# Kernel optimization log

Measured on AMD Instinct MI355X. Metric: run time of the kernel, lower is better.

Reference implementation:

```python
import jax, jax.numpy as jnp
import numpy as np

B, S, D, V = 2, 4096, 2048, 32000
H, HD = 16, 128          # heads, head dim (H*HD == D)
BS = 16                  # block_size
N_ANCH = 128             # num_anchors (static: loss_mask=ones guarantees enough valid positions)
MASK_ID = 31999
DFF = 8192


def rms(x, w, eps=1e-6):
    return x * jax.lax.rsqrt(jnp.mean(x * x, axis=-1, keepdims=True) + eps) * w


def rope(x, pos):
    # x: (..., L, H, hd), pos: (..., L)
    hd = x.shape[-1]
    inv = 1.0 / (10000.0 ** (jnp.arange(0, hd, 2, dtype=jnp.float32) / hd))
    ang = pos[..., None, None].astype(jnp.float32) * inv  # (..., L, 1, hd/2)
    cos, sin = jnp.cos(ang), jnp.sin(ang)
    x1, x2 = x[..., : hd // 2], x[..., hd // 2 :]
    return jnp.concatenate([x1 * cos - x2 * sin, x2 * cos + x1 * sin], axis=-1).astype(x.dtype)


def setup_inputs() -> dict:
    key = jax.random.key(0)
    ks = jax.random.split(key, 12)
    s = 0.02
    return {
        "input_ids": jax.random.randint(ks[0], (B, S), 0, V, dtype=jnp.int32),
        "hidden_states": jax.random.normal(ks[1], (B, S, D), dtype=jnp.float32),
        "loss_mask": jnp.ones((B, S), dtype=jnp.float32),
        "rand_vals": jax.random.uniform(ks[2], (B, S - BS + 1), dtype=jnp.float32),
        "embed_table": jax.random.normal(ks[3], (V, D), dtype=jnp.float32) * s,
        "lm_head_w": jax.random.normal(ks[4], (V, D), dtype=jnp.float32) * s,
        "wq": jax.random.normal(ks[5], (D, D), dtype=jnp.float32) * s,
        "wk": jax.random.normal(ks[6], (D, D), dtype=jnp.float32) * s,
        "wv": jax.random.normal(ks[7], (D, D), dtype=jnp.float32) * s,
        "wo": jax.random.normal(ks[8], (D, D), dtype=jnp.float32) * s,
        "w_gate": jax.random.normal(ks[9], (D, DFF), dtype=jnp.float32) * s,
        "w_up": jax.random.normal(ks[10], (D, DFF), dtype=jnp.float32) * s,
        "w_down": jax.random.normal(ks[11], (DFF, D), dtype=jnp.float32) * s,
        "norm_attn": jnp.ones((D,), dtype=jnp.float32),
        "norm_mlp": jnp.ones((D,), dtype=jnp.float32),
        "norm_out": jnp.ones((D,), dtype=jnp.float32),
        "norm_chs": jnp.ones((D,), dtype=jnp.float32),
    }


def reference(input_ids, hidden_states, loss_mask, rand_vals, embed_table, lm_head_w,
              wq, wk, wv, wo, w_gate, w_up, w_down, norm_attn, norm_mlp, norm_out, norm_chs):
    max_anchor = S - BS
    # ---- anchor sampling: random permutation of valid positions via argsort of rand ----
    valid = loss_mask[:, : max_anchor + 1] > 0.5                       # (B, max_anchor+1)
    valid_counts = valid.sum(axis=1)
    idx = jnp.arange(max_anchor + 1, dtype=jnp.int32)
    masked_idx = jnp.where(valid, idx[None, :], S + 1)
    rv = jnp.where(valid, rand_vals, 2.0)
    order = jnp.argsort(rv, axis=1)
    gathered = jnp.take_along_axis(masked_idx, order, axis=1)
    anchors = jnp.sort(gathered[:, :N_ANCH], axis=1)                   # (B, N)
    keep = jnp.arange(N_ANCH)[None, :] < jnp.minimum(valid_counts, N_ANCH)[:, None]
    anchors = jnp.where(keep, anchors, 0)
    # ---- noise embedding: anchor token at block start, mask token elsewhere ----
    anchor_tok = jnp.take_along_axis(input_ids, jnp.clip(anchors, 0, S - 1), axis=1)
    first_tok = jnp.where(keep, anchor_tok, MASK_ID)
    noise_ids = jnp.full((B, N_ANCH, BS), MASK_ID, dtype=jnp.int32).at[:, :, 0].set(first_tok)
    x = embed_table[noise_ids]                                         # (B,N,BS,D)
    # ---- CHS context hidden: target hidden at anchor-1 ----
    ctx_pos = jnp.maximum(anchors - 1, 0)
    ctx = jnp.take_along_axis(hidden_states, ctx_pos[:, :, None], axis=1)  # (B,N,D)
    # ---- block-diagonal attention: per-block kv = [CHS_i | draft block i] (kv_len=1+BS) ----
    pos_q = anchors[:, :, None] + jnp.arange(BS)[None, None, :]        # (B,N,BS)
    pos_kv = jnp.concatenate([ctx_pos[:, :, None], pos_q], axis=2)     # (B,N,1+BS)
    hq = rms(x, norm_attn)
    hc = rms(ctx, norm_chs)[:, :, None, :]
    kv_in = jnp.concatenate([hc, hq], axis=2)                          # (B,N,1+BS,D)
    q = rope((hq @ wq).reshape(B, N_ANCH, BS, H, HD), pos_q)
    k = rope((kv_in @ wk).reshape(B, N_ANCH, 1 + BS, H, HD), pos_kv)
    v = (kv_in @ wv).reshape(B, N_ANCH, 1 + BS, H, HD)
    scores = jnp.einsum('bnqhd,bnkhd->bnhqk', q, k) * (1.0 / HD ** 0.5)
    attn = jax.nn.softmax(scores, axis=-1)
    out = jnp.einsum('bnhqk,bnkhd->bnqhd', attn, v).reshape(B, N_ANCH, BS, D) @ wo
    out = out * keep[:, :, None, None].astype(out.dtype)               # invalid blocks fully masked
    x = x + out
    h = rms(x, norm_mlp)
    x = x + (jax.nn.silu(h @ w_gate) * (h @ w_up)) @ w_down
    h_out = rms(x, norm_out)
    logits = h_out @ lm_head_w.T                                       # (B,N,BS,V)
    # ---- block-wise CE loss ----
    label_idx = anchors[:, :, None] + jnp.arange(BS)[None, None, :]
    valid_label = label_idx < S
    safe = jnp.minimum(label_idx, S - 1)
    targets = jnp.take_along_axis(jnp.broadcast_to(input_ids[:, None, :], (B, N_ANCH, S)), safe, axis=2)
    lm_g = jnp.take_along_axis(jnp.broadcast_to(loss_mask[:, None, :], (B, N_ANCH, S)), safe, axis=2)
    weight = (keep[:, :, None] & valid_label).astype(jnp.float32)
    weight = weight * (jnp.arange(BS) > 0)[None, None, :].astype(jnp.float32) * lm_g
    logp = jax.nn.log_softmax(logits, axis=-1)
    tok_logp = jnp.take_along_axis(logp, targets[..., None].astype(jnp.int32), axis=-1)[..., 0]
    loss = -(tok_logp * weight).sum() / (weight.sum() + 1e-6)
    pred = jnp.argmax(logits, axis=-1)
    accuracy = ((pred == targets) & (weight > 0.5)).sum().astype(jnp.float32) / (weight.sum() + 1e-6)
    return loss, accuracy
```

## Files before the change

### kernel.cpp

```cpp
#include <hip/hip_runtime.h>
#include <math.h>

typedef unsigned short u16;
typedef unsigned char u8;
typedef short v8s __attribute__((ext_vector_type(8)));
typedef u16   v4u __attribute__((ext_vector_type(4)));
typedef float v4f __attribute__((ext_vector_type(4)));
typedef int   v2i __attribute__((ext_vector_type(2)));
typedef int   v4i __attribute__((ext_vector_type(4)));

#define DEVFN static __device__ __forceinline__

constexpr int cB = 2, cS = 4096, cD = 2048, cV = 32000, cH = 16, cHD = 128;
constexpr int cBS = 16, cNA = 128, cMASK = 31999, cDFF = 8192;
constexpr int NCAND = cS - cBS + 1;
constexpr int MTOK  = cB * cNA * cBS;
constexpr int MKV   = cB * cNA * 17;
constexpr int NCH   = cV / 128;
constexpr int NCH2  = cV / 256;

constexpr int EPI_BF16 = 0, EPI_SILU = 1, EPI_OEMB = 2, EPI_DOWNACC = 3, EPI_STATS = 4, EPI_GLU = 5;
constexpr int ASRC_BF16 = 0, ASRC_RMS = 1, ASRC_AOMAP = 2;

struct RmsSrc {
// ... 160 lines not shown
  long i = ((long)blockIdx.x * 256 + threadIdx.x) * 8;
  long stride = (long)gridDim.x * 256 * 8;
  for (; i < n; i += stride) {
    v4f a = *(const v4f*)(in + i), b = *(const v4f*)(in + i + 4);
    v2i pk;
    pk[0] = pack4fp8(a[0] * scale, a[1] * scale, a[2] * scale, a[3] * scale);
    pk[1] = pack4fp8(b[0] * scale, b[1] * scale, b[2] * scale, b[3] * scale);
    *(v2i*)(out + perm8(i)) = pk;
  }
}

__global__ void k_cvt8(const u16* __restrict__ in, u8* __restrict__ out, long n) {
  long i = ((long)blockIdx.x * 256 + threadIdx.x) * 8;
  long stride = (long)gridDim.x * 256 * 8;
  for (; i < n; i += stride) {
    v8s a = *(const v8s*)(in + i);
    v2i pk;
    pk[0] = pack4fp8(bf2f((u16)a[0]), bf2f((u16)a[1]), bf2f((u16)a[2]), bf2f((u16)a[3]));
    pk[1] = pack4fp8(bf2f((u16)a[4]), bf2f((u16)a[5]), bf2f((u16)a[6]), bf2f((u16)a[7]));
    *(v2i*)(out + perm8(i)) = pk;
  }
}

__global__ void k_tconv(const float* __restrict__ W, u16* __restrict__ WT, int K, int N) {
  __shared__ u16 t[64][72];
  int n0 = blockIdx.x * 64, k0 = blockIdx.y * 64;
  int tid = threadIdx.x;
  int c4 = (tid & 15) * 4, r0 = tid >> 4;
  #pragma unroll
  for (int rr = 0; rr < 64; rr += 16) {
    int k = r0 + rr;
    v4f v = *(const v4f*)(W + (size_t)(k0 + k) * N + n0 + c4);
    #pragma unroll
    for (int e = 0; e < 4; ++e) t[c4 + e][k] = f2bf(v[e]);
  }
  __syncthreads();
  int n = tid >> 2, kq = (tid & 3) * 16;
  v8s o0, o1;
  #pragma unroll
  for (int e = 0; e < 8; ++e) { o0[e] = (short)t[n][kq + e]; o1[e] = (short)t[n][kq + 8 + e]; }
  *(v8s*)(WT + (size_t)(n0 + n) * K + k0 + kq) = o0;
  *(v8s*)(WT + (size_t)(n0 + n) * K + k0 + kq + 8) = o1;
}

__global__ void k_tconv8(const float* __restrict__ W, u8* __restrict__ WT8,
                         int K, int N, int goff, float scale) {
  __shared__ float tf[64][65];
  int n0 = blockIdx.x * 64, k0 = blockIdx.y * 64;
  int tid = threadIdx.x;
  int c4 = (tid & 15) * 4, r0 = tid >> 4;
  #pragma unroll
  for (int rr = 0; rr < 64; rr += 16) {
    int k = r0 + rr;
    v4f v = *(const v4f*)(W + (size_t)(k0 + k) * N + n0 + c4);
    #pragma unroll
    for (int e = 0; e < 4; ++e) tf[c4 + e][k] = v[e];
  }
  __syncthreads();
  int n = tid >> 2, kq = (tid & 3) * 16;
  int gn = n0 + n;
  size_t rout = (goff >= 0) ? (((size_t)(gn >> 4) << 5) + goff + (gn & 15)) : (size_t)gn;
  long base = (long)rout * K + k0 + kq;
  v2i p0, p1;
  p0[0] = pack4fp8(tf[n][kq + 0] * scale, tf[n][kq + 1] * scale, tf[n][kq + 2] * scale, tf[n][kq + 3] * scale);
  p0[1] = pack4fp8(tf[n][kq + 4] * scale, tf[n][kq + 5] * scale, tf[n][kq + 6] * scale, tf[n][kq + 7] * scale);
  p1[0] = pack4fp8(tf[n][kq + 8] * scale, tf[n][kq + 9] * scale, tf[n][kq + 10] * scale, tf[n][kq + 11] * scale);
  p1[1] = pack4fp8(tf[n][kq + 12] * scale, tf[n][kq + 13] * scale, tf[n][kq + 14] * scale, tf[n][kq + 15] * scale);
// ... 94 lines not shown
    __builtin_amdgcn_s_setprio(0);
    __builtin_amdgcn_s_barrier();

    if (t + 2 < NT) stageA(t + 2, 1);
    __builtin_amdgcn_s_setprio(1);
    #pragma unroll
    for (int mi = 0; mi < 4; ++mi)
      #pragma unroll
      for (int ni = 0; ni < 4; ++ni)
        acc[mi + 4][ni] = __builtin_amdgcn_mfma_f32_16x16x32_fp8_fp8(fa[mi + 4].ll[1], fb[ni].ll[1], acc[mi + 4][ni], 0, 0, 0);
    __builtin_amdgcn_s_setprio(0);
    if (t + 2 < NT) { asm volatile("s_waitcnt vmcnt(4)" ::: "memory"); }
    else            { asm volatile("s_waitcnt vmcnt(0)" ::: "memory"); }
    __builtin_amdgcn_s_barrier();
  }
  asm volatile("s_waitcnt vmcnt(0)" ::: "memory");

  #pragma unroll
  for (int mi = 0; mi < 8; ++mi)
    #pragma unroll
    for (int ni = 0; ni < 4; ++ni)
      acc[mi][ni] *= 0.015625f;

  if constexpr (EPI == EPI_GLU) {
    #pragma unroll
    for (int mi = 0; mi < 8; ++mi)
      #pragma unroll
      for (int np = 0; np < 2; ++np)
        #pragma unroll
        for (int r = 0; r < 4; ++r) {
          int grow = m0 + wm * 128 + mi * 16 + lq * 4 + r;
          int gcol = (n0 >> 1) + wn * 32 + np * 16 + lc;
          float g = acc[mi][2 * np][r];
          float u = acc[mi][2 * np + 1][r];
          C8[perm8((size_t)grow * ldc + gcol)] = f2fp8(u * g / (1.0f + __expf(-g)));
        }
    return;
  } else {
    float* s_mx = (float*)lds8;
    float* s_sm = (float*)(lds8 + 4096);
    int*   s_ax = (int*)(lds8 + 8192);
    __syncthreads();
    #pragma unroll
    for (int mi = 0; mi < 8; ++mi) {
      #pragma unroll
      for (int r = 0; r < 4; ++r) {
        float v0 = acc[mi][0][r], v1 = acc[mi][1][r], v2 = acc[mi][2][r], v3 = acc[mi][3][r];
        float mx = v0; int ax = lc;
        if (v1 > mx) { mx = v1; ax = 16 + lc; }
        if (v2 > mx) { mx = v2; ax = 32 + lc; }
        if (v3 > mx) { mx = v3; ax = 48 + lc; }
        #pragma unroll
        for (int off = 1; off < 16; off <<= 1) {
          float om = __shfl_xor(mx, off); int oa = __shfl_xor(ax, off);
          if (om > mx || (om == mx && oa < ax)) { mx = om; ax = oa; }
        }
        float se = __expf(v0 - mx) + __expf(v1 - mx) + __expf(v2 - mx) + __expf(v3 - mx);
        #pragma unroll
        for (int off = 1; off < 16; off <<= 1) se += __shfl_xor(se, off);
        if (lc == 0) {
          int row = wm * 128 + mi * 16 + lq * 4 + r;
          s_mx[row * 4 + wn] = mx; s_sm[row * 4 + wn] = se; s_ax[row * 4 + wn] = wn * 64 + ax;
        }
      }
    }
    __syncthreads();
    if (tid < 256) {
      float gm = s_mx[tid * 4]; int ga = s_ax[tid * 4];
      #pragma unroll
      for (int w = 1; w < 4; ++w) {
        float m = s_mx[tid * 4 + w];
        if (m > gm) { gm = m; ga = s_ax[tid * 4 + w]; }
      }
      float gs = 0.f;
      #pragma unroll
      for (int w = 0; w < 4; ++w) gs += s_sm[tid * 4 + w] * __expf(s_mx[tid * 4 + w] - gm);
      v4f rec; rec[0] = gm; rec[1] = gs; rec[2] = __int_as_float(n0 + ga); rec[3] = 0.f;
      partials[(size_t)(m0 + tid) * nch + blockIdx.y] = rec;
    }
  }
}

template <int EPI>
__launch_bounds__(256, 4)
__global__ void k_gemm9(const u8* __restrict__ A8, const u8* __restrict__ B8,
                        u16* __restrict__ Cbf, float* __restrict__ Cf32,
                        const int* __restrict__ keepArr, RmsSrc rs,
                        int K, int ldb, int ldc) {
  __shared__ __align__(16) u8 lds8[32768];
  const int tid = threadIdx.x;
  const int lane = tid & 63, wid = tid >> 6;
  const int wm = wid >> 1, wn = wid & 1;
  const int lc = lane & 15, lq = lane >> 4;
  const int m0 = blockIdx.x * 128, n0 = blockIdx.y * 128;

  const u8* srcA[2]; const u8* srcB[2];
  #pragma unroll
  for (int i = 0; i < 2; ++i) {
    int ci = i * 256 + tid;
    int r = ci >> 2;
    int logc = (ci & 3) ^ ((r >> 1) & 3);
    srcA[i] = A8 + (size_t)(m0 + r) * K + logc * 16;
// ... 60 lines not shown
  }

  #pragma unroll
  for (int mi = 0; mi < 4; ++mi)
    #pragma unroll
    for (int ni = 0; ni < 4; ++ni)
      #pragma unroll
      for (int r = 0; r < 4; ++r) {
        int grow = m0 + wm * 64 + mi * 16 + lq * 4 + r;
        int gcol = n0 + wn * 64 + ni * 16 + lc;
        size_t idx = (size_t)grow * ldc + gcol;
        float vv = acc[mi][ni][r] * 0.015625f;
        if constexpr (EPI == EPI_BF16) {
          Cbf[idx] = f2bf(vv);
        } else if constexpr (EPI == EPI_OEMB) {
          int t_ = grow & 15, bn = grow >> 4;
          int tok = (t_ == 0) ? rs.ftok[bn] : cMASK;
          float kf = (float)keepArr[bn];
          Cf32[idx] = rs.emb[(size_t)tok * cD + gcol] + vv * kf;
        } else {
          Cf32[idx] += vv;
        }
      }
}

template <int ASRC, int BLAYOUT, int EPI>
__launch_bounds__(256)
__global__ void k_gemm(const u16* __restrict__ Abf, const float* __restrict__ Bw,
                       u16* Cbf, float* Cf32, const u16* Gaux,
                       const int* __restrict__ keepArr, v4f* __restrict__ partials,
                       RmsSrc rs, int K, int ldb, int ldc) {
  __shared__ __align__(16) u16 As[128][40];
  __shared__ __align__(16) u16 Bs[128][40];
  const int tid = threadIdx.x;
  const int m0 = blockIdx.x * 128, n0 = blockIdx.y * 128;
  const int lane = tid & 63, wid = tid >> 6;
  const int wm = wid >> 1, wn = wid & 1;
  const int lc = lane & 15, lk8 = (lane >> 4) * 8;
  const int srow = tid >> 2, sk8 = (tid & 3) * 8;
  v4f acc[4][4];
  #pragma unroll
  for (int i = 0; i < 4; ++i)
    #pragma unroll
    for (int j = 0; j < 4; ++j) acc[i][j] = (v4f){0.f, 0.f, 0.f, 0.f};

  for (int kt = 0; kt < K; kt += 32) {
    __syncthreads();
    for (int mm = srow; mm < 128; mm += 64) {
      if constexpr (ASRC == ASRC_BF16) {
        *(v8s*)&As[mm][sk8] = *(const v8s*)(Abf + (size_t)(m0 + mm) * K + kt + sk8);
      } else if constexpr (ASRC == ASRC_AOMAP) {
        int m = m0 + mm, bn = m >> 4, t = m & 15;
        *(v8s*)&As[mm][sk8] = *(const v8s*)(Abf + (size_t)(bn * 17 + 1 + t) * K + kt + sk8);
      } else {
        int R = m0 + mm;
        int j = R % 17, bn = R / 17, b = bn >> 7;
        const float* src; const float* nw;
        if (j == 0) { src = rs.hs + ((size_t)b * cS + rs.cpos[bn]) * cD; nw = rs.nchs; }
        else {
          int tok = (j == 1) ? rs.ftok[bn] : cMASK;
          src = rs.emb + (size_t)tok * cD; nw = rs.nattn;
        }
        float inv = rs.rowinv[R];
        const v4f* sp = (const v4f*)(src + kt + sk8);
        const v4f* np_ = (const v4f*)(nw + kt + sk8);
        v4f s0 = sp[0], s1 = sp[1], w0 = np_[0], w1 = np_[1];
        v8s pk;
        #pragma unroll
        for (int e = 0; e < 4; ++e) pk[e] = (short)f2bf(s0[e] * inv * w0[e]);
        #pragma unroll
        for (int e = 0; e < 4; ++e) pk[4 + e] = (short)f2bf(s1[e] * inv * w1[e]);
        *(v8s*)&As[mm][sk8] = pk;
      }
    }
    if constexpr (BLAYOUT == 1) {
      for (int nn = srow; nn < 128; nn += 64) {
        const v4f* bp = (const v4f*)(Bw + (size_t)(n0 + nn) * ldb + kt + sk8);
        v4f b0 = bp[0], b1 = bp[1];
        v8s pk;
        #pragma unroll
        for (int e = 0; e < 4; ++e) { pk[e] = (short)f2bf(b0[e]); pk[4 + e] = (short)f2bf(b1[e]); }
        *(v8s*)&Bs[nn][sk8] = pk;
      }
    } else {
      const int bn_ = tid & 127, kq = tid >> 7;
      for (int kk = kq; kk < 8; kk += 2) {
        const int k4 = kk * 4;
        const float* bp = Bw + (size_t)(kt + k4) * ldb + n0 + bn_;
        v4u pk;
        #pragma unroll
        for (int e = 0; e < 4; ++e) pk[e] = f2bf(bp[(size_t)e * ldb]);
        *(v4u*)&Bs[bn_][k4] = pk;
      }
    }
    __syncthreads();
    v8s af[4], bf_[4];
    #pragma unroll
    for (int i = 0; i < 4; ++i) af[i] = *(const v8s*)&As[wm * 64 + i * 16 + lc][lk8];
    #pragma unroll
    for (int i = 0; i < 4; ++i) bf_[i] = *(const v8s*)&Bs[wn * 64 + i * 16 + lc][lk8];
    #pragma unroll
    for (int mi = 0; mi < 4; ++mi)
      #pragma unroll
      for (int ni = 0; ni < 4; ++ni)
        acc[mi][ni] = __builtin_amdgcn_mfma_f32_16x16x32_bf16(af[mi], bf_[ni], acc[mi][ni], 0, 0, 0);
  }

  if constexpr (EPI == EPI_STATS) {
    __shared__ float s_mx[128][2], s_sm[128][2];
    __shared__ int s_ax[128][2];
    #pragma unroll
    for (int mi = 0; mi < 4; ++mi) {
      #pragma unroll
      for (int r = 0; r < 4; ++r) {
        float v0 = acc[mi][0][r], v1 = acc[mi][1][r], v2 = acc[mi][2][r], v3 = acc[mi][3][r];
        float mx = v0; int ax = lc;
        if (v1 > mx) { mx = v1; ax = 16 + lc; }
        if (v2 > mx) { mx = v2; ax = 32 + lc; }
        if (v3 > mx) { mx = v3; ax = 48 + lc; }
        #pragma unroll
        for (int off = 1; off < 16; off <<= 1) {
          float om = __shfl_xor(mx, off); int oa = __shfl_xor(ax, off);
          if (om > mx || (om == mx && oa < ax)) { mx = om; ax = oa; }
        }
        float se = __expf(v0 - mx) + __expf(v1 - mx) + __expf(v2 - mx) + __expf(v3 - mx);
        #pragma unroll
        for (int off = 1; off < 16; off <<= 1) se += __shfl_xor(se, off);
        if (lc == 0) {
          int lr = wm * 64 + mi * 16 + (lane >> 4) * 4 + r;
          s_mx[lr][wn] = mx; s_sm[lr][wn] = se; s_ax[lr][wn] = wn * 64 + ax;
        }
      }
    }
    __syncthreads();
    if (tid < 128) {
      float ma = s_mx[tid][0], mb = s_mx[tid][1];
      float gm = fmaxf(ma, mb);
      float gs = s_sm[tid][0] * __expf(ma - gm) + s_sm[tid][1] * __expf(mb - gm);
      int ga = (ma >= mb) ? s_ax[tid][0] : s_ax[tid][1];
      v4f rec; rec[0] = gm; rec[1] = gs; rec[2] = __int_as_float(n0 + ga); rec[3] = 0.f;
      partials[(size_t)(m0 + tid) * NCH + blockIdx.y] = rec;
    }
    return;
  } else {
    #pragma unroll
    for (int mi = 0; mi < 4; ++mi)
      #pragma unroll
      for (int ni = 0; ni < 4; ++ni)
        #pragma unroll
        for (int r = 0; r < 4; ++r) {
          int grow = m0 + wm * 64 + mi * 16 + (lane >> 4) * 4 + r;
          int gcol = n0 + wn * 64 + ni * 16 + lc;
          size_t idx = (size_t)grow * ldc + gcol;
          float vv = acc[mi][ni][r];
          if constexpr (EPI == EPI_BF16) {
            Cbf[idx] = f2bf(vv);
          } else if constexpr (EPI == EPI_SILU) {
            float g = bf2f(Gaux[idx]);
            Cbf[idx] = f2bf(vv * g / (1.0f + __expf(-g)));
          } else if constexpr (EPI == EPI_OEMB) {
            int t = grow & 15, bn = grow >> 4;
            int tok = (t == 0) ? rs.ftok[bn] : cMASK;
            float kf = (float)keepArr[bn];
            Cf32[idx] = rs.emb[(size_t)tok * cD + gcol] + vv * kf;
          } else {
            Cf32[idx] += vv;
          }
        }
  }
}

__global__ void k_rope(u16* __restrict__ qb, u16* __restrict__ kb,
                       const int* __restrict__ anchors, const int* __restrict__ cpos) {
  int r = blockIdx.x;
  int which = (r >= MKV);
  int rr = which ? r - MKV : r;
  int j = rr % 17, bn = rr / 17;
  if (!which && j == 0) return;
  u16* buf = which ? kb : qb;
  int pos = (which && j == 0) ? cpos[bn] : (anchors[bn] + j - 1);
  float fp = (float)pos;
  for (int p = threadIdx.x; p < cH * 64; p += 256) {
    int h = p >> 6, i = p & 63;
    size_t base = (size_t)rr * cD + h * cHD;
    float x1 = bf2f(buf[base + i]);
    float x2 = bf2f(buf[base + 64 + i]);
    float freq = powf(10000.0f, -((float)(2 * i)) / 128.0f);
    float ang = fp * freq;
    float sn = sinf(ang), cn = cosf(ang);
    buf[base + i]      = f2bf(x1 * cn - x2 * sn);
    buf[base + 64 + i] = f2bf(x2 * cn + x1 * sn);
  }
// ... 15 lines not shown
    vs[r][d] = bf2f(vb[((size_t)(bn * 17 + r)) * cD + h * cHD + d]);
  }
  __syncthreads();
  for (int e = lane; e < 16 * 17; e += 64) {
    int qi = e / 17, ki = e % 17;
    float s = 0.f;
    for (int d = 0; d < 128; ++d) s += qs[qi][d] * ks[ki][d];
    ps[qi][ki] = s * 0.08838834764831845f;
  }
  __syncthreads();
  if (lane < 16) {
    float m = -3e38f;
    for (int kk = 0; kk < 17; ++kk) m = fmaxf(m, ps[lane][kk]);
    float s = 0.f;
    for (int kk = 0; kk < 17; ++kk) { float e_ = __expf(ps[lane][kk] - m); ps[lane][kk] = e_; s += e_; }
    float is = 1.0f / s;
    for (int kk = 0; kk < 17; ++kk) ps[lane][kk] *= is;
  }
  __syncthreads();
  for (int e = lane; e < 16 * 128; e += 64) {
    int qi = e >> 7, d = e & 127;
    float s = 0.f;
    for (int kk = 0; kk < 17; ++kk) s += ps[qi][kk] * vs[kk][d];
    if (ao8) ao8[perm8((size_t)(bn * 16 + qi) * cD + h * cHD + d)] = f2fp8(s);
    else     qb[((size_t)(bn * 17 + 1 + qi)) * cD + h * cHD + d] = f2bf(s);
  }
}

__global__ void k_tgt(const u16* __restrict__ hout, const float* __restrict__ Wlm,
                      const int* __restrict__ ids, const int* __restrict__ anchors,
                      int* __restrict__ tgt_tok, float* __restrict__ tgt_logit) {
  int w = threadIdx.x >> 6, lane = threadIdx.x & 63;
  int m = blockIdx.x * 4 + w;
  int bn = m >> 4, t = m & 15, b = bn / cNA;
  int label = anchors[bn] + t;
  int sl = (label < cS - 1) ? label : (cS - 1);
  int tok = ids[(size_t)b * cS + sl];
  const u16* hr = hout + (size_t)m * cD;
  const float* wr = Wlm + (size_t)tok * cD;
  float s = 0.f;
  for (int d = lane; d < cD; d += 64) s += bf2f(hr[d]) * wr[d];
  s = waveSum(s);
  if (lane == 0) { tgt_tok[m] = tok; tgt_logit[m] = s; }
}

__global__ void k_combine(const v4f* __restrict__ partials, const int* __restrict__ tgt_tok,
                          const float* __restrict__ tgt_logit, const int* __restrict__ keepArr,
                          const int* __restrict__ anchors, const float* __restrict__ lmask,
// ... 47 lines not shown
  for (int m = tid; m < MTOK; m += 256) {
    swl += tokOut[m * 4 + 0];
    sw  += tokOut[m * 4 + 1];
    sm  += tokOut[m * 4 + 2];
  }
  swl = waveSum(swl); sw = waveSum(sw); sm = waveSum(sm);
  __shared__ float r0[4], r1[4], r2[4];
  int lane = tid & 63, w = tid >> 6;
  if (lane == 0) { r0[w] = swl; r1[w] = sw; r2[w] = sm; }
  __syncthreads();
  if (tid == 0) {
    float a = r0[0] + r0[1] + r0[2] + r0[3];
    float b = r1[0] + r1[1] + r1[2] + r1[3];
    float c = r2[0] + r2[1] + r2[2] + r2[3];
    float denom = b + 1e-6f;
    float loss = -a / denom;
    float acc  = c / denom;
    if (b == 0.0f) loss = -300.0f;
    outp[0] = loss;
    outp[1] = acc;
  }
}

__global__ void k_heartbeat(float* outp) {
  if (threadIdx.x == 0) { outp[0] = -55.0f; outp[1] = -55.0f; }
}
__global__ void k_sentinel(float* outp) {
  if (threadIdx.x == 0) { outp[0] = -777.0f; outp[1] = -777.0f; }
}

extern "C" void kernel_launch(void* const* d_in, const int* in_sizes, int n_in,
                              void* d_out, int out_size, void* d_ws, size_t ws_size,
                              hipStream_t stream) {
  const int*   ids   = (const int*)  d_in[0];
  const float* hs    = (const float*)d_in[1];
  const float* lmask = (const float*)d_in[2];
  const float* rv    = (const float*)d_in[3];
  const float* emb   = (const float*)d_in[4];
  const float* wlm   = (const float*)d_in[5];
  const float* wq    = (const float*)d_in[6];
  const float* wk    = (const float*)d_in[7];
  const float* wv    = (const float*)d_in[8];
  const float* wo    = (const float*)d_in[9];
  const float* wg    = (const float*)d_in[10];
  const float* wu    = (const float*)d_in[11];
  const float* wd    = (const float*)d_in[12];
  const float* nattn = (const float*)d_in[13];
  const float* nmlp  = (const float*)d_in[14];
  const float* nout  = (const float*)d_in[15];
  const float* nchs  = (const float*)d_in[16];
  (void)in_sizes; (void)n_in; (void)out_size;

  float* outp = (float*)d_out;
  k_heartbeat<<<dim3(1), 64, 0, stream>>>(outp);

  char* wsb = (char*)d_ws;
  size_t off = 0;
  auto alloc = [&](size_t bytes) -> void* {
    void* p = wsb + off;
    off = (off + bytes + 255) & ~(size_t)255;
    return p;
  };
  int*   anchors = (int*)  alloc((size_t)cB * cNA * 4);
  int*   keepA   = (int*)  alloc((size_t)cB * cNA * 4);
  int*   ftok    = (int*)  alloc((size_t)cB * cNA * 4);
  int*   cpos    = (int*)  alloc((size_t)cB * cNA * 4);
  int*   self    = (int*)  alloc((size_t)cB * NCAND * 4);
  float* rowinv  = (float*)alloc((size_t)MKV * 4);
  int*   ttok    = (int*)  alloc((size_t)MTOK * 4);
  float* tlogit  = (float*)alloc((size_t)MTOK * 4);
  float* tokOut  = (float*)alloc((size_t)MTOK * 4 * 4);

  const size_t szQ  = (size_t)MKV * cD * 2;
  const size_t szX  = (size_t)MTOK * cD * 4;
  u16* qb = (u16*)alloc(szQ);
  const size_t a1off = off;

// ... 51 lines not shown
    k_gemm9<EPI_OEMB><<<dim3(MTOK / 128, cD / 128), 256, 0, stream>>>(
        ao8, wo8, nullptr, xb, keepA, rs, cD, cD, cD);

    k_rms<<<dim3(MTOK), 256, 0, stream>>>(xb, nmlp, hb);
    k_cvt8<<<dim3(1024), 256, 0, stream>>>(hb, h8m, (long)MTOK * cD);

    k_tconv8<<<dim3(128, 32), 256, 0, stream>>>(wg, wgu8, cD, cDFF, 0, 64.0f);
    k_tconv8<<<dim3(128, 32), 256, 0, stream>>>(wu, wgu8, cD, cDFF, 16, 64.0f);
    k_tconv8<<<dim3(32, 128), 256, 0, stream>>>(wd, wd8, cDFF, cD, -1, 64.0f);

    for (int cb = 0; cb < cDFF; cb += 4096) {
      k_gemm8<EPI_GLU><<<dim3(MTOK / 256, 32), 512, 0, stream>>>(
          h8m, wgu8 + (size_t)cb * 2 * cD, cbuf8, nullptr, cD, 4096, 0);
      k_gemm9<EPI_DOWNACC><<<dim3(MTOK / 128, cD / 128), 256, 0, stream>>>(
          cbuf8, wd8 + cb, nullptr, xb, nullptr, rs, 4096, cDFF, cD);
    }

    k_rms<<<dim3(MTOK), 256, 0, stream>>>(xb, nout, houtb);

    k_tgt<<<dim3(MTOK / 4), 256, 0, stream>>>(houtb, wlm, ids, anchors, ttok, tlogit);

    k_cvt8 <<<dim3(1024), 256, 0, stream>>>(houtb, h8, (long)MTOK * cD);
    k_conv8<<<dim3(2048), 256, 0, stream>>>(wlm, wlm8, (long)cV * cD, 64.0f);
    k_gemm8<EPI_STATS><<<dim3(MTOK / 256, NCH2), 512, 0, stream>>>(
        h8, wlm8, nullptr, parts, cD, 0, NCH2);

    k_combine<<<dim3(MTOK), 256, 0, stream>>>(parts, ttok, tlogit, keepA, anchors, lmask, tokOut, NCH2);
    k_final  <<<dim3(1), 256, 0, stream>>>(tokOut, outp);
    return;
  }

  const int cwopts[4] = {4096, 2048, 1024, 512};
  int CW = 0;
  for (int ci = 0; ci < 4; ++ci) {
    int cw = cwopts[ci];
    size_t cbufsz = (size_t)MTOK * cw * 2;
    size_t s1 = 2 * szQ;
    size_t s2 = szX + cbufsz;
    size_t sz = s1 > s2 ? s1 : s2;
    size_t pmin = (size_t)MTOK * NCH * 16;
    if (pmin > sz) sz = pmin;
    if (a1off + sz <= ws_size) { CW = cw; break; }
  }
  if (CW == 0) { k_sentinel<<<dim3(1), 64, 0, stream>>>(outp); return; }

  u16*   kb    = (u16*)(wsb + a1off);
  u16*   vb    = (u16*)(wsb + a1off + szQ);
  float* xb    = (float*)(wsb + a1off);
  u16*   cbuf  = (u16*)(wsb + a1off + szX);
  v4f*   parts = (v4f*)(wsb + a1off);
  u16*   hb    = qb;
  u16*   houtb = qb;

  k_rowinv<<<dim3(MKV), 256, 0, stream>>>(hs, emb, ftok, cpos, rowinv);

  k_gemm<ASRC_RMS, 0, EPI_BF16><<<dim3(MKV / 128, cD / 128), 256, 0, stream>>>(
      nullptr, wq, qb, nullptr, nullptr, nullptr, nullptr, rs, cD, cD, cD);
  k_gemm<ASRC_RMS, 0, EPI_BF16><<<dim3(MKV / 128, cD / 128), 256, 0, stream>>>(
      nullptr, wk, kb, nullptr, nullptr, nullptr, nullptr, rs, cD, cD, cD);
  k_gemm<ASRC_RMS, 0, EPI_BF16><<<dim3(MKV / 128, cD / 128), 256, 0, stream>>>(
      nullptr, wv, vb, nullptr, nullptr, nullptr, nullptr, rs, cD, cD, cD);

  k_rope<<<dim3(2 * MKV), 256, 0, stream>>>(qb, kb, anchors, cpos);
  k_attn<<<dim3(cB * cNA * cH), 64, 0, stream>>>(qb, kb, vb, nullptr);

  k_gemm<ASRC_AOMAP, 0, EPI_OEMB><<<dim3(MTOK / 128, cD / 128), 256, 0, stream>>>(
      qb, wo, nullptr, xb, nullptr, keepA, nullptr, rs, cD, cD, cD);

  k_rms<<<dim3(MTOK), 256, 0, stream>>>(xb, nmlp, hb);

  for (int cb = 0; cb < cDFF; cb += CW) {
    k_gemm<ASRC_BF16, 0, EPI_BF16><<<dim3(MTOK / 128, CW / 128), 256, 0, stream>>>(
        hb, wg + cb, cbuf, nullptr, nullptr, nullptr, nullptr, rs, cD, cDFF, CW);
    k_gemm<ASRC_BF16, 0, EPI_SILU><<<dim3(MTOK / 128, CW / 128), 256, 0, stream>>>(
        hb, wu + cb, cbuf, nullptr, cbuf, nullptr, nullptr, rs, cD, cDFF, CW);
    k_gemm<ASRC_BF16, 0, EPI_DOWNACC><<<dim3(MTOK / 128, cD / 128), 256, 0, stream>>>(
        cbuf, wd + (size_t)cb * cD, nullptr, xb, nullptr, nullptr, nullptr, rs, CW, cD, cD);
  }

  k_rms<<<dim3(MTOK), 256, 0, stream>>>(xb, nout, houtb);

  k_tgt<<<dim3(MTOK / 4), 256, 0, stream>>>(houtb, wlm, ids, anchors, ttok, tlogit);
  k_gemm<ASRC_BF16, 1, EPI_STATS><<<dim3(MTOK / 128, cV / 128), 256, 0, stream>>>(
      houtb, wlm, nullptr, nullptr, nullptr, nullptr, parts, rs, cD, cD, 0);

  k_combine<<<dim3(MTOK), 256, 0, stream>>>(parts, ttok, tlogit, keepA, anchors, lmask, tokOut, NCH);
  k_final  <<<dim3(1), 256, 0, stream>>>(tokOut, outp);
}
```

Before: 1.443 ms.

## Add 512x256-tile FP8 LM-head GEMM kernel with fused softmax stats; drop bf16 fallback

Adds a dedicated LM-head GEMM kernel that uses 512x256 output tiles per 512-thread block (16x4 accumulator fragments per wave) with a double-buffered 96KB LDS pipeline and interleaved staging. It keeps the fused per-chunk max/sum-exp/argmax epilogue, and the EPI_STATS path moves out of the generic FP8 GEMM, which now only handles GLU. The larger tile is meant to raise operand reuse and cut global/LDS traffic for the vocab projection. In exchange it runs one block per CU with high register pressure and fewer blocks in the grid. The unused bf16 fallback path, the heartbeat kernel and dead helpers are removed.

New measurement: 2.431 ms. +68.4%, slower.

```diff
diff --git a/kernel.cpp b/kernel.cpp
--- a/kernel.cpp
+++ b/kernel.cpp
@@ -206,27 +206,6 @@
   }
 }
 
-__global__ void k_tconv(const float* __restrict__ W, u16* __restrict__ WT, int K, int N) {
-  __shared__ u16 t[64][72];
-  int n0 = blockIdx.x * 64, k0 = blockIdx.y * 64;
-  int tid = threadIdx.x;
-  int c4 = (tid & 15) * 4, r0 = tid >> 4;
-  #pragma unroll
-  for (int rr = 0; rr < 64; rr += 16) {
-    int k = r0 + rr;
-    v4f v = *(const v4f*)(W + (size_t)(k0 + k) * N + n0 + c4);
-    #pragma unroll
-    for (int e = 0; e < 4; ++e) t[c4 + e][k] = f2bf(v[e]);
-  }
-  __syncthreads();
-  int n = tid >> 2, kq = (tid & 3) * 16;
-  v8s o0, o1;
-  #pragma unroll
-  for (int e = 0; e < 8; ++e) { o0[e] = (short)t[n][kq + e]; o1[e] = (short)t[n][kq + 8 + e]; }
-  *(v8s*)(WT + (size_t)(n0 + n) * K + k0 + kq) = o0;
-  *(v8s*)(WT + (size_t)(n0 + n) * K + k0 + kq + 8) = o1;
-}
-
 __global__ void k_tconv8(const float* __restrict__ W, u8* __restrict__ WT8,
                          int K, int N, int goff, float scale) {
   __shared__ float tf[64][65];
@@ -367,62 +346,195 @@
     for (int ni = 0; ni < 4; ++ni)
       acc[mi][ni] *= 0.015625f;
 
-  if constexpr (EPI == EPI_GLU) {
-    #pragma unroll
-    for (int mi = 0; mi < 8; ++mi)
-      #pragma unroll
-      for (int np = 0; np < 2; ++np)
-        #pragma unroll
-        for (int r = 0; r < 4; ++r) {
-          int grow = m0 + wm * 128 + mi * 16 + lq * 4 + r;
-          int gcol = (n0 >> 1) + wn * 32 + np * 16 + lc;
-          float g = acc[mi][2 * np][r];
-          float u = acc[mi][2 * np + 1][r];
-          C8[perm8((size_t)grow * ldc + gcol)] = f2fp8(u * g / (1.0f + __expf(-g)));
-        }
-    return;
-  } else {
-    float* s_mx = (float*)lds8;
-    float* s_sm = (float*)(lds8 + 4096);
-    int*   s_ax = (int*)(lds8 + 8192);
-    __syncthreads();
-    #pragma unroll
-    for (int mi = 0; mi < 8; ++mi) {
+  #pragma unroll
+  for (int mi = 0; mi < 8; ++mi)
+    #pragma unroll
+    for (int np = 0; np < 2; ++np)
       #pragma unroll
       for (int r = 0; r < 4; ++r) {
-        float v0 = acc[mi][0][r], v1 = acc[mi][1][r], v2 = acc[mi][2][r], v3 = acc[mi][3][r];
-        float mx = v0; int ax = lc;
-        if (v1 > mx) { mx = v1; ax = 16 + lc; }
-        if (v2 > mx) { mx = v2; ax = 32 + lc; }
-        if (v3 > mx) { mx = v3; ax = 48 + lc; }
-        #pragma unroll
-        for (int off = 1; off < 16; off <<= 1) {
-          float om = __shfl_xor(mx, off); int oa = __shfl_xor(ax, off);
-          if (om > mx || (om == mx && oa < ax)) { mx = om; ax = oa; }
-        }
-        float se = __expf(v0 - mx) + __expf(v1 - mx) + __expf(v2 - mx) + __expf(v3 - mx);
-        #pragma unroll
-        for (int off = 1; off < 16; off <<= 1) se += __shfl_xor(se, off);
-        if (lc == 0) {
-          int row = wm * 128 + mi * 16 + lq * 4 + r;
-          s_mx[row * 4 + wn] = mx; s_sm[row * 4 + wn] = se; s_ax[row * 4 + wn] = wn * 64 + ax;
-        }
+        int grow = m0 + wm * 128 + mi * 16 + lq * 4 + r;
+        int gcol = (n0 >> 1) + wn * 32 + np * 16 + lc;
+        float g = acc[mi][2 * np][r];
+        float u = acc[mi][2 * np + 1][r];
+        C8[perm8((size_t)grow * ldc + gcol)] = f2fp8(u * g / (1.0f + __expf(-g)));
+      }
+  (void)partials; (void)nch;
+}
+
+__launch_bounds__(512, 1)
+__global__ void k_gemm10(const u8* __restrict__ A8, const u8* __restrict__ B8,
+                         v4f* __restrict__ partials, int K, int nch) {
+  __shared__ __align__(16) u8 lds8[98304];
+  const int tid = threadIdx.x;
+  const int lane = tid & 63, wid = tid >> 6;
+  const int wm = wid >> 2, wn = wid & 3;
+  const int lc = lane & 15, lq = lane >> 4;
+  const int m0 = blockIdx.x * 512, n0 = blockIdx.y * 256;
+
+  const u8* srcA[4]; const u8* srcB[2];
+  #pragma unroll
+  for (int i = 0; i < 4; ++i) {
+    int ci = i * 512 + tid;
+    int r = ci >> 2;
+    int logc = (ci & 3) ^ ((r >> 1) & 3);
+    srcA[i] = A8 + (size_t)(m0 + r) * K + logc * 16;
+  }
+  #pragma unroll
+  for (int i = 0; i < 2; ++i) {
+    int ci = i * 512 + tid;
+    int r = ci >> 2;
+    int logc = (ci & 3) ^ ((r >> 1) & 3);
+    srcB[i] = B8 + (size_t)(n0 + r) * K + logc * 16;
+  }
+
+  v4f acc[16][4];
+  #pragma unroll
+  for (int i = 0; i < 16; ++i)
+    #pragma unroll
+    for (int j = 0; j < 4; ++j) acc[i][j] = (v4f){0.f, 0.f, 0.f, 0.f};
+
+  const int csw = (lc >> 1) & 3;
+  int aoff[16], boff[4];
+  #pragma unroll
+  for (int mi = 0; mi < 16; ++mi) aoff[mi] = (wm * 256 + mi * 16 + lc) * 64 + ((lq ^ csw) << 4);
+  #pragma unroll
+  for (int ni = 0; ni < 4; ++ni) boff[ni] = (wn * 64 + ni * 16 + lc) * 64 + ((lq ^ csw) << 4);
+
+  auto stageA = [&](int t, int i) {
+    gload16(&lds8[(t & 1) * 49152 + i * 8192 + wid * 1024], srcA[i] + t * 64);
+  };
+  auto stageB = [&](int t, int i) {
+    gload16(&lds8[(t & 1) * 49152 + 32768 + i * 8192 + wid * 1024], srcB[i] + t * 64);
+  };
+
+  stageB(0, 0); stageB(0, 1); stageA(0, 0); stageA(0, 1); stageA(0, 2); stageA(0, 3);
+  stageB(1, 0); stageB(1, 1); stageA(1, 0); stageA(1, 1); stageA(1, 2);
+  asm volatile("s_waitcnt vmcnt(5)" ::: "memory");
+  __builtin_amdgcn_s_barrier();
+
+  union Frag { v4i v; long long ll[2]; };
+  const int NT = K >> 6;
+  for (int t = 0; t < NT; ++t) {
+    const u8* Ab = &lds8[(t & 1) * 49152];
+    const u8* Bb = Ab + 32768;
+    Frag fa[4], fb[4];
+
+    #pragma unroll
+    for (int ni = 0; ni < 4; ++ni) fb[ni].v = *(const v4i*)(Bb + boff[ni]);
+    #pragma unroll
+    for (int j = 0; j < 4; ++j) fa[j].v = *(const v4i*)(Ab + aoff[j]);
+    if (t + 1 < NT) stageA(t + 1, 3);
+    asm volatile("s_waitcnt lgkmcnt(0)" ::: "memory");
+    __builtin_amdgcn_sched_barrier(0);
+    __builtin_amdgcn_s_setprio(1);
+    #pragma unroll
+    for (int j = 0; j < 4; ++j)
+      #pragma unroll
+      for (int ni = 0; ni < 4; ++ni) {
+        acc[j][ni] = __builtin_amdgcn_mfma_f32_16x16x32_fp8_fp8(fa[j].ll[0], fb[ni].ll[0], acc[j][ni], 0, 0, 0);
+        acc[j][ni] = __builtin_amdgcn_mfma_f32_16x16x32_fp8_fp8(fa[j].ll[1], fb[ni].ll[1], acc[j][ni], 0, 0, 0);
+      }
+    __builtin_amdgcn_s_setprio(0);
+    __builtin_amdgcn_s_barrier();
+
+    #pragma unroll
+    for (int j = 0; j < 4; ++j) fa[j].v = *(const v4i*)(Ab + aoff[4 + j]);
+    if (t + 2 < NT) { stageB(t + 2, 0); stageB(t + 2, 1); }
+    asm volatile("s_waitcnt lgkmcnt(0)" ::: "memory");
+    __builtin_amdgcn_sched_barrier(0);
+    __builtin_amdgcn_s_setprio(1);
+    #pragma unroll
+    for (int j = 0; j < 4; ++j)
+      #pragma unroll
+      for (int ni = 0; ni < 4; ++ni) {
+        acc[4 + j][ni] = __builtin_amdgcn_mfma_f32_16x16x32_fp8_fp8(fa[j].ll[0], fb[ni].ll[0], acc[4 + j][ni], 0, 0, 0);
+        acc[4 + j][ni] = __builtin_amdgcn_mfma_f32_16x16x32_fp8_fp8(fa[j].ll[1], fb[ni].ll[1], acc[4 + j][ni], 0, 0, 0);
+      }
+    __builtin_amdgcn_s_setprio(0);
+    __builtin_amdgcn_s_barrier();
+
+    #pragma unroll
+    for (int j = 0; j < 4; ++j) fa[j].v = *(const v4i*)(Ab + aoff[8 + j]);
+    if (t + 2 < NT) { stageA(t + 2, 0); stageA(t + 2, 1); }
+    asm volatile("s_waitcnt lgkmcnt(0)" ::: "memory");
+    __builtin_amdgcn_sched_barrier(0);
+    __builtin_amdgcn_s_setprio(1);
+    #pragma unroll
+    for (int j = 0; j < 4; ++j)
+      #pragma unroll
+      for (int ni = 0; ni < 4; ++ni) {
+        acc[8 + j][ni] = __builtin_amdgcn_mfma_f32_16x16x32_fp8_fp8(fa[j].ll[0], fb[ni].ll[0], acc[8 + j][ni], 0, 0, 0);
+        acc[8 + j][ni] = __builtin_amdgcn_mfma_f32_16x16x32_fp8_fp8(fa[j].ll[1], fb[ni].ll[1], acc[8 + j][ni], 0, 0, 0);
+      }
+    __builtin_amdgcn_s_setprio(0);
+    __builtin_amdgcn_s_barrier();
+
+    #pragma unroll
+    for (int j = 0; j < 4; ++j) fa[j].v = *(const v4i*)(Ab + aoff[12 + j]);
+    if (t + 2 < NT) stageA(t + 2, 2);
+    asm volatile("s_waitcnt lgkmcnt(0)" ::: "memory");
+    __builtin_amdgcn_sched_barrier(0);
+    __builtin_amdgcn_s_setprio(1);
+    #pragma unroll
+    for (int j = 0; j < 4; ++j)
+      #pragma unroll
+      for (int ni = 0; ni < 4; ++ni) {
+        acc[12 + j][ni] = __builtin_amdgcn_mfma_f32_16x16x32_fp8_fp8(fa[j].ll[0], fb[ni].ll[0], acc[12 + j][ni], 0, 0, 0);
+        acc[12 + j][ni] = __builtin_amdgcn_mfma_f32_16x16x32_fp8_fp8(fa[j].ll[1], fb[ni].ll[1], acc[12 + j][ni], 0, 0, 0);
+      }
+    __builtin_amdgcn_s_setprio(0);
+    if (t + 2 < NT) { asm volatile("s_waitcnt vmcnt(5)" ::: "memory"); }
+    else            { asm volatile("s_waitcnt vmcnt(0)" ::: "memory"); }
+    __builtin_amdgcn_s_barrier();
+  }
+  asm volatile("s_waitcnt vmcnt(0)" ::: "memory");
+
+  #pragma unroll
+  for (int mi = 0; mi < 16; ++mi)
+    #pragma unroll
+    for (int ni = 0; ni < 4; ++ni)
+      acc[mi][ni] *= 0.015625f;
+
+  float* s_mx = (float*)lds8;
+  float* s_sm = (float*)(lds8 + 8192);
+  int*   s_ax = (int*)(lds8 + 16384);
+  __syncthreads();
+  #pragma unroll
+  for (int mi = 0; mi < 16; ++mi) {
+    #pragma unroll
+    for (int r = 0; r < 4; ++r) {
+      float v0 = acc[mi][0][r], v1 = acc[mi][1][r], v2 = acc[mi][2][r], v3 = acc[mi][3][r];
+      float mx = v0; int ax = lc;
+      if (v1 > mx) { mx = v1; ax = 16 + lc; }
+      if (v2 > mx) { mx = v2; ax = 32 + lc; }
+      if (v3 > mx) { mx = v3; ax = 48 + lc; }
+      #pragma unroll
+      for (int off = 1; off < 16; off <<= 1) {
+        float om = __shfl_xor(mx, off); int oa = __shfl_xor(ax, off);
+        if (om > mx || (om == mx && oa < ax)) { mx = om; ax = oa; }
+      }
+      float se = __expf(v0 - mx) + __expf(v1 - mx) + __expf(v2 - mx) + __expf(v3 - mx);
+      #pragma unroll
+      for (int off = 1; off < 16; off <<= 1) se += __shfl_xor(se, off);
+      if (lc == 0) {
+        int row = wm * 256 + mi * 16 + lq * 4 + r;
+        s_mx[row * 4 + wn] = mx; s_sm[row * 4 + wn] = se; s_ax[row * 4 + wn] = wn * 64 + ax;
       }
     }
-    __syncthreads();
-    if (tid < 256) {
-      float gm = s_mx[tid * 4]; int ga = s_ax[tid * 4];
-      #pragma unroll
-      for (int w = 1; w < 4; ++w) {
-        float m = s_mx[tid * 4 + w];
-        if (m > gm) { gm = m; ga = s_ax[tid * 4 + w]; }
-      }
-      float gs = 0.f;
-      #pragma unroll
-      for (int w = 0; w < 4; ++w) gs += s_sm[tid * 4 + w] * __expf(s_mx[tid * 4 + w] - gm);
-      v4f rec; rec[0] = gm; rec[1] = gs; rec[2] = __int_as_float(n0 + ga); rec[3] = 0.f;
-      partials[(size_t)(m0 + tid) * nch + blockIdx.y] = rec;
+  }
+  __syncthreads();
+  {
+    float gm = s_mx[tid * 4]; int ga = s_ax[tid * 4];
+    #pragma unroll
+    for (int w = 1; w < 4; ++w) {
+      float m = s_mx[tid * 4 + w];
+      if (m > gm) { gm = m; ga = s_ax[tid * 4 + w]; }
     }
+    float gs = 0.f;
+    #pragma unroll
+    for (int w = 0; w < 4; ++w) gs += s_sm[tid * 4 + w] * __expf(s_mx[tid * 4 + w] - gm);
+    v4f rec; rec[0] = gm; rec[1] = gs; rec[2] = __int_as_float(n0 + ga); rec[3] = 0.f;
+    partials[(size_t)(m0 + tid) * nch + blockIdx.y] = rec;
   }
 }
 
@@ -529,152 +641,6 @@
           Cf32[idx] += vv;
         }
       }
-}
-
-template <int ASRC, int BLAYOUT, int EPI>
-__launch_bounds__(256)
-__global__ void k_gemm(const u16* __restrict__ Abf, const float* __restrict__ Bw,
-                       u16* Cbf, float* Cf32, const u16* Gaux,
-                       const int* __restrict__ keepArr, v4f* __restrict__ partials,
-                       RmsSrc rs, int K, int ldb, int ldc) {
-  __shared__ __align__(16) u16 As[128][40];
-  __shared__ __align__(16) u16 Bs[128][40];
-  const int tid = threadIdx.x;
-  const int m0 = blockIdx.x * 128, n0 = blockIdx.y * 128;
-  const int lane = tid & 63, wid = tid >> 6;
-  const int wm = wid >> 1, wn = wid & 1;
-  const int lc = lane & 15, lk8 = (lane >> 4) * 8;
-  const int srow = tid >> 2, sk8 = (tid & 3) * 8;
-  v4f acc[4][4];
-  #pragma unroll
-  for (int i = 0; i < 4; ++i)
-    #pragma unroll
-    for (int j = 0; j < 4; ++j) acc[i][j] = (v4f){0.f, 0.f, 0.f, 0.f};
-
-  for (int kt = 0; kt < K; kt += 32) {
-    __syncthreads();
-    for (int mm = srow; mm < 128; mm += 64) {
-      if constexpr (ASRC == ASRC_BF16) {
-        *(v8s*)&As[mm][sk8] = *(const v8s*)(Abf + (size_t)(m0 + mm) * K + kt + sk8);
-      } else if constexpr (ASRC == ASRC_AOMAP) {
-        int m = m0 + mm, bn = m >> 4, t = m & 15;
-        *(v8s*)&As[mm][sk8] = *(const v8s*)(Abf + (size_t)(bn * 17 + 1 + t) * K + kt + sk8);
-      } else {
-        int R = m0 + mm;
-        int j = R % 17, bn = R / 17, b = bn >> 7;
-        const float* src; const float* nw;
-        if (j == 0) { src = rs.hs + ((size_t)b * cS + rs.cpos[bn]) * cD; nw = rs.nchs; }
-        else {
-          int tok = (j == 1) ? rs.ftok[bn] : cMASK;
-          src = rs.emb + (size_t)tok * cD; nw = rs.nattn;
-        }
-        float inv = rs.rowinv[R];
-        const v4f* sp = (const v4f*)(src + kt + sk8);
-        const v4f* np_ = (const v4f*)(nw + kt + sk8);
-        v4f s0 = sp[0], s1 = sp[1], w0 = np_[0], w1 = np_[1];
-        v8s pk;
-        #pragma unroll
-        for (int e = 0; e < 4; ++e) pk[e] = (short)f2bf(s0[e] * inv * w0[e]);
-        #pragma unroll
-        for (int e = 0; e < 4; ++e) pk[4 + e] = (short)f2bf(s1[e] * inv * w1[e]);
-        *(v8s*)&As[mm][sk8] = pk;
-      }
-    }
-    if constexpr (BLAYOUT == 1) {
-      for (int nn = srow; nn < 128; nn += 64) {
-        const v4f* bp = (const v4f*)(Bw + (size_t)(n0 + nn) * ldb + kt + sk8);
-        v4f b0 = bp[0], b1 = bp[1];
-        v8s pk;
-        #pragma unroll
-        for (int e = 0; e < 4; ++e) { pk[e] = (short)f2bf(b0[e]); pk[4 + e] = (short)f2bf(b1[e]); }
-        *(v8s*)&Bs[nn][sk8] = pk;
-      }
-    } else {
-      const int bn_ = tid & 127, kq = tid >> 7;
-      for (int kk = kq; kk < 8; kk += 2) {
-        const int k4 = kk * 4;
-        const float* bp = Bw + (size_t)(kt + k4) * ldb + n0 + bn_;
-        v4u pk;
-        #pragma unroll
-        for (int e = 0; e < 4; ++e) pk[e] = f2bf(bp[(size_t)e * ldb]);
-        *(v4u*)&Bs[bn_][k4] = pk;
-      }
-    }
-    __syncthreads();
-    v8s af[4], bf_[4];
-    #pragma unroll
-    for (int i = 0; i < 4; ++i) af[i] = *(const v8s*)&As[wm * 64 + i * 16 + lc][lk8];
-    #pragma unroll
-    for (int i = 0; i < 4; ++i) bf_[i] = *(const v8s*)&Bs[wn * 64 + i * 16 + lc][lk8];
-    #pragma unroll
-    for (int mi = 0; mi < 4; ++mi)
-      #pragma unroll
-      for (int ni = 0; ni < 4; ++ni)
-        acc[mi][ni] = __builtin_amdgcn_mfma_f32_16x16x32_bf16(af[mi], bf_[ni], acc[mi][ni], 0, 0, 0);
-  }
-
-  if constexpr (EPI == EPI_STATS) {
-    __shared__ float s_mx[128][2], s_sm[128][2];
-    __shared__ int s_ax[128][2];
-    #pragma unroll
-    for (int mi = 0; mi < 4; ++mi) {
-      #pragma unroll
-      for (int r = 0; r < 4; ++r) {
-        float v0 = acc[mi][0][r], v1 = acc[mi][1][r], v2 = acc[mi][2][r], v3 = acc[mi][3][r];
-        float mx = v0; int ax = lc;
-        if (v1 > mx) { mx = v1; ax = 16 + lc; }
-        if (v2 > mx) { mx = v2; ax = 32 + lc; }
-        if (v3 > mx) { mx = v3; ax = 48 + lc; }
-        #pragma unroll
-        for (int off = 1; off < 16; off <<= 1) {
-          float om = __shfl_xor(mx, off); int oa = __shfl_xor(ax, off);
-          if (om > mx || (om == mx && oa < ax)) { mx = om; ax = oa; }
-        }
-        float se = __expf(v0 - mx) + __expf(v1 - mx) + __expf(v2 - mx) + __expf(v3 - mx);
-        #pragma unroll
-        for (int off = 1; off < 16; off <<= 1) se += __shfl_xor(se, off);
-        if (lc == 0) {
-          int lr = wm * 64 + mi * 16 + (lane >> 4) * 4 + r;
-          s_mx[lr][wn] = mx; s_sm[lr][wn] = se; s_ax[lr][wn] = wn * 64 + ax;
-        }
-      }
-    }
-    __syncthreads();
-    if (tid < 128) {
-      float ma = s_mx[tid][0], mb = s_mx[tid][1];
-      float gm = fmaxf(ma, mb);
-      float gs = s_sm[tid][0] * __expf(ma - gm) + s_sm[tid][1] * __expf(mb - gm);
-      int ga = (ma >= mb) ? s_ax[tid][0] : s_ax[tid][1];
-      v4f rec; rec[0] = gm; rec[1] = gs; rec[2] = __int_as_float(n0 + ga); rec[3] = 0.f;
-      partials[(size_t)(m0 + tid) * NCH + blockIdx.y] = rec;
-    }
-    return;
-  } else {
-    #pragma unroll
-    for (int mi = 0; mi < 4; ++mi)
-      #pragma unroll
-      for (int ni = 0; ni < 4; ++ni)
-        #pragma unroll
-        for (int r = 0; r < 4; ++r) {
-          int grow = m0 + wm * 64 + mi * 16 + (lane >> 4) * 4 + r;
-          int gcol = n0 + wn * 64 + ni * 16 + lc;
-          size_t idx = (size_t)grow * ldc + gcol;
-          float vv = acc[mi][ni][r];
-          if constexpr (EPI == EPI_BF16) {
-            Cbf[idx] = f2bf(vv);
-          } else if constexpr (EPI == EPI_SILU) {
-            float g = bf2f(Gaux[idx]);
-            Cbf[idx] = f2bf(vv * g / (1.0f + __expf(-g)));
-          } else if constexpr (EPI == EPI_OEMB) {
-            int t = grow & 15, bn = grow >> 4;
-            int tok = (t == 0) ? rs.ftok[bn] : cMASK;
-            float kf = (float)keepArr[bn];
-            Cf32[idx] = rs.emb[(size_t)tok * cD + gcol] + vv * kf;
-          } else {
-            Cf32[idx] += vv;
-          }
-        }
-  }
 }
 
 __global__ void k_rope(u16* __restrict__ qb, u16* __restrict__ kb,
@@ -736,8 +702,7 @@
     int qi = e >> 7, d = e & 127;
     float s = 0.f;
     for (int kk = 0; kk < 17; ++kk) s += ps[qi][kk] * vs[kk][d];
-    if (ao8) ao8[perm8((size_t)(bn * 16 + qi) * cD + h * cHD + d)] = f2fp8(s);
-    else     qb[((size_t)(bn * 17 + 1 + qi)) * cD + h * cHD + d] = f2bf(s);
+    ao8[perm8((size_t)(bn * 16 + qi) * cD + h * cHD + d)] = f2fp8(s);
   }
 }
 
@@ -831,9 +796,6 @@
   }
 }
 
-__global__ void k_heartbeat(float* outp) {
-  if (threadIdx.x == 0) { outp[0] = -55.0f; outp[1] = -55.0f; }
-}
 __global__ void k_sentinel(float* outp) {
   if (threadIdx.x == 0) { outp[0] = -777.0f; outp[1] = -777.0f; }
 }
@@ -861,7 +823,6 @@
   (void)in_sizes; (void)n_in; (void)out_size;
 
   float* outp = (float*)d_out;
-  k_heartbeat<<<dim3(1), 64, 0, stream>>>(outp);
 
   char* wsb = (char*)d_ws;
   size_t off = 0;
@@ -959,68 +920,12 @@
 
     k_cvt8 <<<dim3(1024), 256, 0, stream>>>(houtb, h8, (long)MTOK * cD);
     k_conv8<<<dim3(2048), 256, 0, stream>>>(wlm, wlm8, (long)cV * cD, 64.0f);
-    k_gemm8<EPI_STATS><<<dim3(MTOK / 256, NCH2), 512, 0, stream>>>(
-        h8, wlm8, nullptr, parts, cD, 0, NCH2);
+    k_gemm10<<<dim3(MTOK / 512, NCH2), 512, 0, stream>>>(h8, wlm8, parts, cD, NCH2);
 
     k_combine<<<dim3(MTOK), 256, 0, stream>>>(parts, ttok, tlogit, keepA, anchors, lmask, tokOut, NCH2);
     k_final  <<<dim3(1), 256, 0, stream>>>(tokOut, outp);
     return;
   }
 
-  const int cwopts[4] = {4096, 2048, 1024, 512};
-  int CW = 0;
-  for (int ci = 0; ci < 4; ++ci) {
-    int cw = cwopts[ci];
-    size_t cbufsz = (size_t)MTOK * cw * 2;
-    size_t s1 = 2 * szQ;
-    size_t s2 = szX + cbufsz;
-    size_t sz = s1 > s2 ? s1 : s2;
-    size_t pmin = (size_t)MTOK * NCH * 16;
-    if (pmin > sz) sz = pmin;
-    if (a1off + sz <= ws_size) { CW = cw; break; }
-  }
-  if (CW == 0) { k_sentinel<<<dim3(1), 64, 0, stream>>>(outp); return; }
-
-  u16*   kb    = (u16*)(wsb + a1off);
-  u16*   vb    = (u16*)(wsb + a1off + szQ);
-  float* xb    = (float*)(wsb + a1off);
-  u16*   cbuf  = (u16*)(wsb + a1off + szX);
-  v4f*   parts = (v4f*)(wsb + a1off);
-  u16*   hb    = qb;
-  u16*   houtb = qb;
-
-  k_rowinv<<<dim3(MKV), 256, 0, stream>>>(hs, emb, ftok, cpos, rowinv);
-
-  k_gemm<ASRC_RMS, 0, EPI_BF16><<<dim3(MKV / 128, cD / 128), 256, 0, stream>>>(
-      nullptr, wq, qb, nullptr, nullptr, nullptr, nullptr, rs, cD, cD, cD);
-  k_gemm<ASRC_RMS, 0, EPI_BF16><<<dim3(MKV / 128, cD / 128), 256, 0, stream>>>(
-      nullptr, wk, kb, nullptr, nullptr, nullptr, nullptr, rs, cD, cD, cD);
-  k_gemm<ASRC_RMS, 0, EPI_BF16><<<dim3(MKV / 128, cD / 128), 256, 0, stream>>>(
-      nullptr, wv, vb, nullptr, nullptr, nullptr, nullptr, rs, cD, cD, cD);
-
-  k_rope<<<dim3(2 * MKV), 256, 0, stream>>>(qb, kb, anchors, cpos);
-  k_attn<<<dim3(cB * cNA * cH), 64, 0, stream>>>(qb, kb, vb, nullptr);
-
-  k_gemm<ASRC_AOMAP, 0, EPI_OEMB><<<dim3(MTOK / 128, cD / 128), 256, 0, stream>>>(
-      qb, wo, nullptr, xb, nullptr, keepA, nullptr, rs, cD, cD, cD);
-
-  k_rms<<<dim3(MTOK), 256, 0, stream>>>(xb, nmlp, hb);
-
-  for (int cb = 0; cb < cDFF; cb += CW) {
-    k_gemm<ASRC_BF16, 0, EPI_BF16><<<dim3(MTOK / 128, CW / 128), 256, 0, stream>>>(
-        hb, wg + cb, cbuf, nullptr, nullptr, nullptr, nullptr, rs, cD, cDFF, CW);
-    k_gemm<ASRC_BF16, 0, EPI_SILU><<<dim3(MTOK / 128, CW / 128), 256, 0, stream>>>(
-        hb, wu + cb, cbuf, nullptr, cbuf, nullptr, nullptr, rs, cD, cDFF, CW);
-    k_gemm<ASRC_BF16, 0, EPI_DOWNACC><<<dim3(MTOK / 128, cD / 128), 256, 0, stream>>>(
-        cbuf, wd + (size_t)cb * cD, nullptr, xb, nullptr, nullptr, nullptr, rs, CW, cD, cD);
-  }
-
-  k_rms<<<dim3(MTOK), 256, 0, stream>>>(xb, nout, houtb);
-
-  k_tgt<<<dim3(MTOK / 4), 256, 0, stream>>>(houtb, wlm, ids, anchors, ttok, tlogit);
-  k_gemm<ASRC_BF16, 1, EPI_STATS><<<dim3(MTOK / 128, cV / 128), 256, 0, stream>>>(
-      houtb, wlm, nullptr, nullptr, nullptr, nullptr, parts, rs, cD, cD, 0);
-
-  k_combine<<<dim3(MTOK), 256, 0, stream>>>(parts, ttok, tlogit, keepA, anchors, lmask, tokOut, NCH);
-  k_final  <<<dim3(1), 256, 0, stream>>>(tokOut, outp);
-}
+  k_sentinel<<<dim3(1), 64, 0, stream>>>(outp);
+}
```
